# Kernel tuning notes

Hardware: AMD Instinct MI355X
Metric: run time of the kernel (lower is better)

The kernel has to match this reference:

```python
import jax, jax.numpy as jnp
import numpy as np

B, S, D, H, DQK, DV, DFF, L = 8, 512, 512, 8, 64, 64, 2048, 2
SCALE = float(np.sqrt(DQK))


def sinusoid_pe(s, d):
    pos = jnp.arange(s, dtype=jnp.float32)[:, None]
    div = jnp.exp(jnp.arange(0, d, 2, dtype=jnp.float32) * (-np.log(10000.0) / d))
    pe = jnp.zeros((s, d), jnp.float32)
    pe = pe.at[:, 0::2].set(jnp.sin(pos * div))
    pe = pe.at[:, 1::2].set(jnp.cos(pos * div))
    return pe


def ms_masks(s, steps=(4, 8, 16), rep=2):
    # Vectorized equivalent of multi_scale_mask: window of `step` neighbors,
    # shifted near the boundaries so the total neighbor count stays = step.
    i = jnp.arange(s)[:, None]
    j = jnp.arange(s)[None, :]
    ms = []
    for step in steps:
        s2 = step // 2
        left = jnp.where(i < s // 2, jnp.minimum(i, s2), step - jnp.minimum(s - 1 - i, s2))
        right = step - left
        m = (j >= i - left) & (j <= i + right)
        ms += [m] * rep
    return jnp.stack(ms)  # [6, S, S] bool


def layer_norm(x, g, b):
    mu = x.mean(-1, keepdims=True)
    var = ((x - mu) ** 2).mean(-1, keepdims=True)
    return (x - mu) / jnp.sqrt(var + 1e-6) * g + b


def mha(qin, kin, vin, wq, wk, wv, wo, g, b, mask):
    bq, lq, _ = qin.shape
    lk = kin.shape[1]
    q = (qin @ wq).reshape(bq, lq, H, DQK).transpose(0, 2, 1, 3)  # bhqd
    k = (kin @ wk).reshape(bq, lk, H, DQK).transpose(0, 2, 1, 3)
    v = (vin @ wv).reshape(bq, lk, H, DV).transpose(0, 2, 1, 3)
    scores = jnp.einsum('bhqd,bhkd->bhqk', q / SCALE, k)
    scores = jnp.where(mask, scores, jnp.float32(-1e9))
    p = jax.nn.softmax(scores, axis=-1)
    o = jnp.einsum('bhqk,bhkd->bhqd', p, v).transpose(0, 2, 1, 3).reshape(bq, lq, H * DV)
    return layer_norm(o @ wo + qin, g, b)


def ffn(x, w1, b1, w2, b2, g, bb):
    h = jax.nn.relu(x @ w1 + b1)
    return layer_norm(h @ w2 + b2 + x, g, bb)


def setup_inputs() -> dict:
    key = jax.random.key(0)
    ks = jax.random.split(key, 40)
    it = iter(range(40))
    d = {}
    d['src_seq'] = jax.random.normal(ks[next(it)], (B, S, D), jnp.float32)
    d['trg_seq'] = jax.random.normal(ks[next(it)], (B, S, D), jnp.float32)
    d['enc_pad_num'] = jax.random.randint(ks[next(it)], (B,), 0, 64)
    d['dec_pad_num'] = jax.random.randint(ks[next(it)], (B,), 0, 64)

    def w(shape):
        return jax.random.normal(ks[next(it)], shape, jnp.float32) * 0.02

    for p in ('e_wq', 'e_wk', 'e_wv'):
        d[p] = w((L, D, H * DQK))
    d['e_wo'] = w((L, H * DV, D))
    d['e_g1'] = jnp.ones((L, D)); d['e_b1'] = jnp.zeros((L, D))
    d['e_w1'] = w((L, D, DFF)); d['e_bb1'] = jnp.zeros((L, DFF))
    d['e_w2'] = w((L, DFF, D)); d['e_bb2'] = jnp.zeros((L, D))
    d['e_g2'] = jnp.ones((L, D)); d['e_b2'] = jnp.zeros((L, D))
    for p in ('d_swq', 'd_swk', 'd_swv'):
        d[p] = w((L, D, H * DQK))
    d['d_swo'] = w((L, H * DV, D))
    d['d_g1'] = jnp.ones((L, D)); d['d_b1'] = jnp.zeros((L, D))
    for p in ('d_cwq', 'd_cwk', 'd_cwv'):
        d[p] = w((L, D, H * DQK))
    d['d_cwo'] = w((L, H * DV, D))
    d['d_g2'] = jnp.ones((L, D)); d['d_b2'] = jnp.zeros((L, D))
    d['d_w1'] = w((L, D, DFF)); d['d_bb1'] = jnp.zeros((L, DFF))
    d['d_w2'] = w((L, DFF, D)); d['d_bb2'] = jnp.zeros((L, D))
    d['d_g3'] = jnp.ones((L, D)); d['d_b3'] = jnp.zeros((L, D))
    return d


def reference(src_seq, trg_seq, enc_pad_num, dec_pad_num,
              e_wq, e_wk, e_wv, e_wo, e_g1, e_b1, e_w1, e_bb1, e_w2, e_bb2, e_g2, e_b2,
              d_swq, d_swk, d_swv, d_swo, d_g1, d_b1,
              d_cwq, d_cwk, d_cwv, d_cwo, d_g2, d_b2,
              d_w1, d_bb1, d_w2, d_bb2, d_g3, d_b3):
    ms = ms_masks(S)  # [6, S, S]
    src_pad = jnp.arange(S)[None, :] < (S - enc_pad_num)[:, None]  # [B, S]
    trg_pad = jnp.arange(S)[None, :] < (S - dec_pad_num)[:, None]

    def full_mask(pad):
        base = pad[:, None, None, :]  # [B,1,1,S]
        win = jnp.logical_and(ms[None], base)  # [B,6,S,S]
        dense = jnp.broadcast_to(base, (B, H - ms.shape[0], S, S))
        return jnp.concatenate([win, dense], axis=1)  # [B,H,S,S]

    src_mask = full_mask(src_pad)
    trg_mask = full_mask(trg_pad)
    pe = sinusoid_pe(S, D)

    x = src_seq + pe[None]
    for l in range(L):
        x = mha(x, x, x, e_wq[l], e_wk[l], e_wv[l], e_wo[l], e_g1[l], e_b1[l], src_mask)
        x = ffn(x, e_w1[l], e_bb1[l], e_w2[l], e_bb2[l], e_g2[l], e_b2[l])

    y = trg_seq + pe[None]
    for l in range(L):
        y = mha(y, y, y, d_swq[l], d_swk[l], d_swv[l], d_swo[l], d_g1[l], d_b1[l], trg_mask)
        y = mha(y, x, x, d_cwq[l], d_cwk[l], d_cwv[l], d_cwo[l], d_g2[l], d_b2[l], src_mask)
        y = ffn(y, d_w1[l], d_bb1[l], d_w2[l], d_bb2[l], d_g3[l], d_b3[l])
    return y
```

## Files before the change

kernel.cpp:

```cpp
#include <hip/hip_runtime.h>
#include <hip/hip_bf16.h>

#define BB 8
#define SS 512
#define DD 512
#define HH 8
#define DQKv 64
#define DFFv 2048
#define LL 2

typedef __attribute__((ext_vector_type(8))) __bf16 bf16x8;
typedef __attribute__((ext_vector_type(4))) float f32x4;

static __device__ __forceinline__ ushort f2b(float x) {
    unsigned int u = __float_as_uint(x);
    unsigned int r = (u + 0x7FFFu + ((u >> 16) & 1u)) >> 16;
    return (ushort)r;
}
static __device__ __forceinline__ float b2f(ushort u) {
    return __uint_as_float(((unsigned int)u) << 16);
}

typedef __attribute__((address_space(1))) const unsigned int gas_u32;
typedef __attribute__((address_space(3))) unsigned int las_u32;
static __device__ __forceinline__ void gload16(const void* g, void* l) {
    __builtin_amdgcn_global_load_lds((gas_u32*)g, (las_u32*)l, 16, 0, 0);
}

__global__ __launch_bounds__(256) void add_pe2_k(const float* __restrict__ src,
                                                 const float* __restrict__ trg,
                                                 float* __restrict__ xf,
                                                 ushort* __restrict__ xb,
                                                 float* __restrict__ yf,
                                                 ushort* __restrict__ yb) {
    const int NQ = BB * SS * DD / 4;
    int i = blockIdx.x * 256 + threadIdx.x;
    const bool second = i >= NQ;
    const int ii = second ? i - NQ : i;
    const int rem = ii & (SS * DD / 4 - 1);
    const int d4 = rem & (DD / 4 - 1);
    const int s = rem >> 7;

    float4 a = ((const float4*)(second ? trg : src))[ii];
    const float c = -9.210340371976184f / 512.0f;
    const float div0 = __expf((float)(4 * d4) * c);
    const float div1 = __expf((float)(4 * d4 + 2) * c);
    const float a0 = (float)s * div0, a1 = (float)s * div1;
    a.x += sinf(a0); a.y += cosf(a0);
    a.z += sinf(a1); a.w += cosf(a1);

    float* of = second ? yf : xf;
    ushort* ob = second ? yb : xb;
    ((float4*)of)[ii] = a;
    ushort4 ub;
    ub.x = f2b(a.x); ub.y = f2b(a.y); ub.z = f2b(a.z); ub.w = f2b(a.w);
    ((ushort4*)ob)[ii] = ub;
}

__global__ __launch_bounds__(256) void tcast_k(const float* __restrict__ s0,
                                               const float* __restrict__ s1,
                                               const float* __restrict__ s2,
                                               const float* __restrict__ s3,
                                               ushort* __restrict__ dst,
                                               int K, int N) {
    __shared__ ushort st[64][72];
    const float* src = (blockIdx.z == 0) ? s0 : (blockIdx.z == 1) ? s1
                     : (blockIdx.z == 2) ? s2 : s3;
    ushort* d = dst + (size_t)blockIdx.z * K * N;
    const int k0 = blockIdx.y * 64, n0 = blockIdx.x * 64;
    const int t = threadIdx.x;
    const int r = t >> 2, c4 = (t & 3) * 16;
#pragma unroll
    for (int i = 0; i < 16; i += 4) {
        float4 v = *(const float4*)&src[(size_t)(k0 + r) * N + n0 + c4 + i];
        st[c4 + i + 0][r] = f2b(v.x);
        st[c4 + i + 1][r] = f2b(v.y);
        st[c4 + i + 2][r] = f2b(v.z);
        st[c4 + i + 3][r] = f2b(v.w);
    }
    __syncthreads();
    const int n = t >> 2, seg = (t & 3) * 16;
    *(uint4*)&d[(size_t)(n0 + n) * K + k0 + seg]     = *(const uint4*)&st[n][seg];
    *(uint4*)&d[(size_t)(n0 + n) * K + k0 + seg + 8] = *(const uint4*)&st[n][seg + 8];
}

#define NW 32
struct WTab {
    const float* src[NW];
    unsigned off[NW];
    int Kd[NW];
    int Nd[NW];
    int cum[NW + 1];
};

__global__ __launch_bounds__(256) void tcast_all_k(WTab tab, ushort* __restrict__ dst) {
    __shared__ ushort st[64][72];
    const int t = blockIdx.x;
    int m = 0;
    while (t >= tab.cum[m + 1]) ++m;
    const int local = t - tab.cum[m];
    const int ntx = tab.Nd[m];
    const int bx = local % ntx, by = local / ntx;
    const float* src = tab.src[m];
    ushort* d = dst + tab.off[m];
    const int N = ntx * 64, K = tab.Kd[m] * 64;
    const int k0 = by * 64, n0 = bx * 64;

    const int tt = threadIdx.x;
    const int r = tt >> 2, c4 = (tt & 3) * 16;
#pragma unroll
    for (int i = 0; i < 16; i += 4) {
        float4 v = *(const float4*)&src[(size_t)(k0 + r) * N + n0 + c4 + i];
        st[c4 + i + 0][r] = f2b(v.x);
        st[c4 + i + 1][r] = f2b(v.y);
        st[c4 + i + 2][r] = f2b(v.z);
        st[c4 + i + 3][r] = f2b(v.w);
    }
    __syncthreads();
    const int n = tt >> 2, seg = (tt & 3) * 16;
    *(uint4*)&d[(size_t)(n0 + n) * K + k0 + seg]     = *(const uint4*)&st[n][seg];
    *(uint4*)&d[(size_t)(n0 + n) * K + k0 + seg + 8] = *(const uint4*)&st[n][seg + 8];
}

template <bool BIAS, bool RES, bool RELU, bool OUTBF>
__global__ __launch_bounds__(256) void gemm2_k(const ushort* __restrict__ A,
                                               const ushort* __restrict__ Bt,
                                               const float* __restrict__ bias,
                                               const float* __restrict__ res,
                                               void* __restrict__ Cout,
                                               int M, int N, int K, int nbx) {
    __shared__ ushort sA[2][64 * 64];
    __shared__ ushort sB[2][64 * 64];

    const int tid = threadIdx.x;
    const int nwg = gridDim.x;
    const int wg = blockIdx.x;
    const int swz = (wg & 7) * (nwg >> 3) + (wg >> 3);
    const int bx = swz % nbx, by = swz / nbx;

    const int lane = tid & 63, w = tid >> 6;
    const int wm = w >> 1, wn = w & 1;
    const int llo = lane & 15, lhi = lane >> 4;

    const int srow = tid >> 3;
    const int scol = (((tid & 7) ^ (srow & 7)) * 8);
    const ushort* Ab = A + (size_t)(by * 64 + srow) * K + scol;
    const ushort* Bb = Bt + (size_t)(bx * 64 + srow) * K + scol;
    const int sOff = srow * 128 + (tid & 7) * 16;

    f32x4 acc[2][2] = {};
    const int nt = K >> 6;

#pragma unroll
    for (int i = 0; i < 2; ++i) {
        gload16(Ab + (size_t)i * 32 * K, (char*)sA[0] + sOff + i * 32 * 128);
        gload16(Bb + (size_t)i * 32 * K, (char*)sB[0] + sOff + i * 32 * 128);
    }
    __syncthreads();

    int cur = 0;
    for (int t = 0; t < nt; ++t) {
        if (t + 1 < nt) {
            const int k0 = (t + 1) << 6;
#pragma unroll
            for (int i = 0; i < 2; ++i) {
                gload16(Ab + (size_t)i * 32 * K + k0, (char*)sA[cur ^ 1] + sOff + i * 32 * 128);
                gload16(Bb + (size_t)i * 32 * K + k0, (char*)sB[cur ^ 1] + sOff + i * 32 * 128);
            }
        }
        const int sw = llo & 7;
#pragma unroll
        for (int ks = 0; ks < 2; ++ks) {
            const int pc = ((ks * 4 + lhi) ^ sw) * 8;
            bf16x8 af[2];
#pragma unroll
            for (int fa = 0; fa < 2; ++fa)
                af[fa] = *(const bf16x8*)&sA[cur][(wm * 32 + fa * 16 + llo) * 64 + pc];
            bf16x8 bfrag[2];
#pragma unroll
            for (int fb = 0; fb < 2; ++fb)
                bfrag[fb] = *(const bf16x8*)&sB[cur][(wn * 32 + fb * 16 + llo) * 64 + pc];
#pragma unroll
            for (int fa = 0; fa < 2; ++fa)
#pragma unroll
                for (int fb = 0; fb < 2; ++fb)
                    acc[fa][fb] = __builtin_amdgcn_mfma_f32_16x16x32_bf16(
                        af[fa], bfrag[fb], acc[fa][fb], 0, 0, 0);
        }
        __syncthreads();
        cur ^= 1;
    }

#pragma unroll
    for (int fa = 0; fa < 2; ++fa) {
#pragma unroll
        for (int fb = 0; fb < 2; ++fb) {
            const int col = bx * 64 + wn * 32 + fb * 16 + llo;
            const float bv = BIAS ? bias[col] : 0.f;
#pragma unroll
            for (int j = 0; j < 4; ++j) {
                const int row = by * 64 + wm * 32 + fa * 16 + lhi * 4 + j;
                float v = acc[fa][fb][j] + bv;
                if (RES) v += res[(size_t)row * N + col];
                if (RELU) v = fmaxf(v, 0.f);
                if (OUTBF) ((ushort*)Cout)[(size_t)row * N + col] = f2b(v);
                else       ((float*)Cout)[(size_t)row * N + col] = v;
            }
        }
    }
}

template <bool BIAS, bool RES, bool RELU, bool OUTBF>
__global__ __launch_bounds__(256) void gemm3_k(const ushort* __restrict__ A,
                                               const ushort* __restrict__ Bt,
                                               const float* __restrict__ bias,
                                               const float* __restrict__ res,
                                               void* __restrict__ Cout,
                                               int M, int N, int K, int nbx) {
    __shared__ ushort sA[2][64 * 64];
    __shared__ ushort sB[2][128 * 64];

    const int tid = threadIdx.x;
    const int nwg = gridDim.x;
    const int wg = blockIdx.x;
    const int swz = (wg & 7) * (nwg >> 3) + (wg >> 3);
    const int bx = swz % nbx, by = swz / nbx;

    const int lane = tid & 63, w = tid >> 6;
    const int wm = w >> 1, wn = w & 1;
    const int llo = lane & 15, lhi = lane >> 4;

    const int srow = tid >> 3;
    const int scol = (((tid & 7) ^ (srow & 7)) * 8);
    const ushort* Ab = A + (size_t)(by * 64 + srow) * K + scol;
    const ushort* Bb = Bt + (size_t)(bx * 128 + srow) * K + scol;
    const int sOff = srow * 128 + (tid & 7) * 16;

    f32x4 acc[2][4] = {};
    const int nt = K >> 6;

#pragma unroll
    for (int i = 0; i < 2; ++i)
        gload16(Ab + (size_t)i * 32 * K, (char*)sA[0] + sOff + i * 32 * 128);
#pragma unroll
    for (int i = 0; i < 4; ++i)
        gload16(Bb + (size_t)i * 32 * K, (char*)sB[0] + sOff + i * 32 * 128);
    __syncthreads();

    int cur = 0;
    for (int t = 0; t < nt; ++t) {
        if (t + 1 < nt) {
            const int k0 = (t + 1) << 6;
#pragma unroll
            for (int i = 0; i < 2; ++i)
                gload16(Ab + (size_t)i * 32 * K + k0, (char*)sA[cur ^ 1] + sOff + i * 32 * 128);
#pragma unroll
            for (int i = 0; i < 4; ++i)
                gload16(Bb + (size_t)i * 32 * K + k0, (char*)sB[cur ^ 1] + sOff + i * 32 * 128);
        }
        const int sw = llo & 7;
#pragma unroll
        for (int ks = 0; ks < 2; ++ks) {
            const int pc = ((ks * 4 + lhi) ^ sw) * 8;
            bf16x8 af[2];
#pragma unroll
            for (int fa = 0; fa < 2; ++fa)
                af[fa] = *(const bf16x8*)&sA[cur][(wm * 32 + fa * 16 + llo) * 64 + pc];
            bf16x8 bfrag[4];
#pragma unroll
            for (int fb = 0; fb < 4; ++fb)
                bfrag[fb] = *(const bf16x8*)&sB[cur][(wn * 64 + fb * 16 + llo) * 64 + pc];
#pragma unroll
            for (int fa = 0; fa < 2; ++fa)
#pragma unroll
                for (int fb = 0; fb < 4; ++fb)
                    acc[fa][fb] = __builtin_amdgcn_mfma_f32_16x16x32_bf16(
                        af[fa], bfrag[fb], acc[fa][fb], 0, 0, 0);
        }
        __syncthreads();
        cur ^= 1;
    }

#pragma unroll
    for (int fa = 0; fa < 2; ++fa) {
#pragma unroll
        for (int fb = 0; fb < 4; ++fb) {
            const int col = bx * 128 + wn * 64 + fb * 16 + llo;
            const float bv = BIAS ? bias[col] : 0.f;
#pragma unroll
            for (int j = 0; j < 4; ++j) {
                const int row = by * 64 + wm * 32 + fa * 16 + lhi * 4 + j;
                float v = acc[fa][fb][j] + bv;
                if (RES) v += res[(size_t)row * N + col];
                if (RELU) v = fmaxf(v, 0.f);
                if (OUTBF) ((ushort*)Cout)[(size_t)row * N + col] = f2b(v);
                else       ((float*)Cout)[(size_t)row * N + col] = v;
            }
        }
    }
}

__global__ __launch_bounds__(256) void attn_k(const ushort* __restrict__ QKV,
                                              ushort* __restrict__ O,
                                              const int* __restrict__ pad) {
    __shared__ ushort sQ[64][72];
    __shared__ ushort sK[64][72];
    __shared__ ushort sVt[64][72];
    __shared__ ushort sP[64][72];

    const int tid = threadIdx.x;
    const int b = blockIdx.z, h = blockIdx.y, q0 = blockIdx.x << 6;
    const int klim = SS - pad[b];
    const int lane = tid & 63, w = tid >> 6;
    const int qw0 = w << 4;
    const int lhi = lane >> 4, llo = lane & 15;
    const int ST = 3 * DD;

    {
        const int r = tid >> 2, seg = (tid & 3) << 4;
        const ushort* src = &QKV[(size_t)(b * SS + q0 + r) * ST + h * DQKv + seg];
        *(uint4*)&sQ[r][seg]     = *(const uint4*)src;
        *(uint4*)&sQ[r][seg + 8] = *(const uint4*)(src + 8);
    }

    auto window = [&](int i, int& wlo, int& whi) {
        if (h < 6) {
            const int step = 4 << (h >> 1);
            const int s2 = step >> 1;
            const int a1 = (i < s2) ? i : s2;
            const int a2 = ((SS - 1 - i) < s2) ? (SS - 1 - i) : s2;
            const int left = (i < SS / 2) ? a1 : (step - a2);
            wlo = i - left;
            whi = wlo + step;
        } else {
            wlo = 0;
            whi = SS - 1;
        }
    };

    int lo[4], hi[4];
#pragma unroll
    for (int j = 0; j < 4; ++j) window(q0 + qw0 + lhi * 4 + j, lo[j], hi[j]);

    int kt0 = 0, kt1 = SS;
    if (h < 6) {
        int lo0, hi0, lo63, hi63;
        window(q0, lo0, hi0);
        window(q0 + 63, lo63, hi63);
        if (lo63 >= klim) {
            kt0 = 0; kt1 = SS;
        } else {
            kt0 = (lo0 >> 6) << 6;
            kt1 = ((hi63 >> 6) + 1) << 6;
            if (kt1 > SS) kt1 = SS;
        }
    }

    float mr[4] = {-1e30f, -1e30f, -1e30f, -1e30f};
    float lr[4] = {0.f, 0.f, 0.f, 0.f};
    f32x4 oacc[4] = {};

    for (int kt = kt0; kt < kt1; kt += 64) {
        __syncthreads();
        {
            const int r = tid >> 2, seg = (tid & 3) << 4;
            const ushort* ksrc = &QKV[(size_t)(b * SS + kt + r) * ST + DD + h * DQKv + seg];
            *(uint4*)&sK[r][seg]     = *(const uint4*)ksrc;
            *(uint4*)&sK[r][seg + 8] = *(const uint4*)(ksrc + 8);
            const ushort* vsrc = &QKV[(size_t)(b * SS + kt + r) * ST + 2 * DD + h * DQKv + seg];
            uint4 u0 = *(const uint4*)vsrc;
            uint4 u1 = *(const uint4*)(vsrc + 8);
            const ushort* v0 = (const ushort*)&u0;
            const ushort* v1 = (const ushort*)&u1;
#pragma unroll
            for (int i = 0; i < 8; ++i) sVt[seg + i][r] = v0[i];
#pragma unroll
            for (int i = 0; i < 8; ++i) sVt[seg + 8 + i][r] = v1[i];
        }
        __syncthreads();

        f32x4 sacc[4] = {};
#pragma unroll
        for (int ks = 0; ks < 2; ++ks) {
            bf16x8 aq = *(const bf16x8*)&sQ[qw0 + llo][ks * 32 + lhi * 8];
#pragma unroll
            for (int n = 0; n < 4; ++n) {
                bf16x8 bk = *(const bf16x8*)&sK[n * 16 + llo][ks * 32 + lhi * 8];
                sacc[n] = __builtin_amdgcn_mfma_f32_16x16x32_bf16(aq, bk, sacc[n], 0, 0, 0);
            }
        }

#pragma unroll
        for (int j = 0; j < 4; ++j) {
            float s[4];
#pragma unroll
            for (int n = 0; n < 4; ++n) {
                const int kidx = kt + n * 16 + llo;
                const bool ok = (kidx < klim) && (kidx >= lo[j]) && (kidx <= hi[j]);
                s[n] = ok ? (sacc[n][j] * 0.125f) : -1e9f;
            }
            float tm = fmaxf(fmaxf(s[0], s[1]), fmaxf(s[2], s[3]));
#pragma unroll
            for (int off = 8; off; off >>= 1) tm = fmaxf(tm, __shfl_xor(tm, off));
            const float mn = fmaxf(mr[j], tm);
            const float alpha = __expf(mr[j] - mn);
            mr[j] = mn;
            float ps = 0.f;
            const int prow = qw0 + lhi * 4 + j;
#pragma unroll
            for (int n = 0; n < 4; ++n) {
                const ushort pb = f2b(__expf(s[n] - mn));
                sP[prow][n * 16 + llo] = pb;
                ps += b2f(pb);
            }
#pragma unroll
            for (int off = 8; off; off >>= 1) ps += __shfl_xor(ps, off);
            lr[j] = lr[j] * alpha + ps;
            oacc[0][j] *= alpha; oacc[1][j] *= alpha;
            oacc[2][j] *= alpha; oacc[3][j] *= alpha;
        }

#pragma unroll
        for (int ks = 0; ks < 2; ++ks) {
            bf16x8 ap = *(const bf16x8*)&sP[qw0 + llo][ks * 32 + lhi * 8];
#pragma unroll
            for (int n = 0; n < 4; ++n) {
                bf16x8 bv = *(const bf16x8*)&sVt[n * 16 + llo][ks * 32 + lhi * 8];
                oacc[n] = __builtin_amdgcn_mfma_f32_16x16x32_bf16(ap, bv, oacc[n], 0, 0, 0);
            }
        }
    }

#pragma unroll
    for (int j = 0; j < 4; ++j) {
        const float inv = 1.f / lr[j];
        const int q = q0 + qw0 + lhi * 4 + j;
#pragma unroll
        for (int n = 0; n < 4; ++n) {
            O[(size_t)(b * SS + q) * (HH * DQKv) + h * DQKv + n * 16 + llo] =
                f2b(oacc[n][j] * inv);
        }
    }
}

__global__ __launch_bounds__(256) void ln_k(const float* __restrict__ in,
                                            const float* __restrict__ g,
                                            const float* __restrict__ bvec,
                                            float* __restrict__ outf,
                                            ushort* __restrict__ outb) {
    const int row = blockIdx.x;
    const int tid = threadIdx.x;
    const float2 xv = *(const float2*)&in[(size_t)row * DD + tid * 2];

    __shared__ float red[4];
    __shared__ float red2[4];
    const int wid = tid >> 6, lane = tid & 63;

    float s = xv.x + xv.y;
#pragma unroll
    for (int off = 32; off; off >>= 1) s += __shfl_xor(s, off);
    if (lane == 0) red[wid] = s;
    __syncthreads();
    const float mu = (red[0] + red[1] + red[2] + red[3]) * (1.f / 512.f);

    const float dx = xv.x - mu, dy = xv.y - mu;
    float q = dx * dx + dy * dy;
#pragma unroll
    for (int off = 32; off; off >>= 1) q += __shfl_xor(q, off);
    if (lane == 0) red2[wid] = q;
    __syncthreads();
    const float var = (red2[0] + red2[1] + red2[2] + red2[3]) * (1.f / 512.f);
    const float rs = rsqrtf(var + 1e-6f);

    float2 o;
    o.x = dx * rs * g[tid * 2] + bvec[tid * 2];
    o.y = dy * rs * g[tid * 2 + 1] + bvec[tid * 2 + 1];
    *(float2*)&outf[(size_t)row * DD + tid * 2] = o;
    ushort2 ub; ub.x = f2b(o.x); ub.y = f2b(o.y);
    *(ushort2*)&outb[(size_t)row * DD + tid * 2] = ub;
}

extern "C" void kernel_launch(void* const* d_in, const int* in_sizes, int n_in,
                              void* d_out, int out_size, void* d_ws, size_t ws_size,
                              hipStream_t stream) {
    const float* src_seq = (const float*)d_in[0];
    const float* trg_seq = (const float*)d_in[1];
    const int* enc_pad = (const int*)d_in[2];
    const int* dec_pad = (const int*)d_in[3];
    const float* e_wq = (const float*)d_in[4];
    const float* e_wk = (const float*)d_in[5];
    const float* e_wv = (const float*)d_in[6];
    const float* e_wo = (const float*)d_in[7];
    const float* e_g1 = (const float*)d_in[8];
    const float* e_b1 = (const float*)d_in[9];
    const float* e_w1 = (const float*)d_in[10];
    const float* e_bb1 = (const float*)d_in[11];
    const float* e_w2 = (const float*)d_in[12];
    const float* e_bb2 = (const float*)d_in[13];
    const float* e_g2 = (const float*)d_in[14];
    const float* e_b2 = (const float*)d_in[15];
    const float* d_swq = (const float*)d_in[16];
    const float* d_swk = (const float*)d_in[17];
    const float* d_swv = (const float*)d_in[18];
    const float* d_swo = (const float*)d_in[19];
    const float* d_g1 = (const float*)d_in[20];
    const float* d_b1 = (const float*)d_in[21];
    const float* d_cwq = (const float*)d_in[22];
    const float* d_cwk = (const float*)d_in[23];
    const float* d_cwv = (const float*)d_in[24];
    const float* d_cwo = (const float*)d_in[25];
    const float* d_g2 = (const float*)d_in[26];
    const float* d_b2 = (const float*)d_in[27];
    const float* d_w1 = (const float*)d_in[28];
    const float* d_bb1 = (const float*)d_in[29];
    const float* d_w2 = (const float*)d_in[30];
    const float* d_bb2 = (const float*)d_in[31];
    const float* d_g3 = (const float*)d_in[32];
    const float* d_b3 = (const float*)d_in[33];
    (void)in_sizes; (void)n_in; (void)out_size;

    const int M = BB * SS;
    const int NTOK = BB * SS * DD;
    const size_t WSZ = (size_t)DD * 512;

    float* ws = (float*)d_ws;
    float* x  = ws;
    float* y  = x + NTOK;
    float* t0 = y + NTOK;
    ushort* xbf  = (ushort*)(t0 + NTOK);
    ushort* ybf  = xbf + NTOK;
    ushort* qkvb = ybf + NTOK;
    ushort* ob   = qkvb + (size_t)M * 1536;
    ushort* hbf  = qkvb;
    ushort* warena = ob + NTOK;

    const float* wsrc[NW]; int wK[NW], wN[NW]; size_t woff[NW];
    int wcnt = 0; size_t acc = 0;
    auto push = [&](const float* p, int K, int N) {
        wsrc[wcnt] = p; wK[wcnt] = K; wN[wcnt] = N; woff[wcnt] = acc;
        acc += (size_t)K * N; ++wcnt;
    };
    for (int l = 0; l < LL; ++l) {
        push(e_wq + (size_t)l * WSZ, 512, 512);
        push(e_wk + (size_t)l * WSZ, 512, 512);
        push(e_wv + (size_t)l * WSZ, 512, 512);
        push(e_wo + (size_t)l * WSZ, 512, 512);
        push(e_w1 + (size_t)l * DD * DFFv, 512, DFFv);
        push(e_w2 + (size_t)l * DFFv * DD, DFFv, 512);
    }
    for (int l = 0; l < LL; ++l) {
        push(d_swq + (size_t)l * WSZ, 512, 512);
        push(d_swk + (size_t)l * WSZ, 512, 512);
        push(d_swv + (size_t)l * WSZ, 512, 512);
        push(d_swo + (size_t)l * WSZ, 512, 512);
        push(d_cwq + (size_t)l * WSZ, 512, 512);
        push(d_cwk + (size_t)l * WSZ, 512, 512);
        push(d_cwv + (size_t)l * WSZ, 512, 512);
        push(d_cwo + (size_t)l * WSZ, 512, 512);
        push(d_w1 + (size_t)l * DD * DFFv, 512, DFFv);
        push(d_w2 + (size_t)l * DFFv * DD, DFFv, 512);
    }

    const size_t base_bytes = (size_t)(warena - (ushort*)d_ws) * 2;
    const bool big = ws_size >= base_bytes + acc * 2;

    if (big) {
        WTab tab;
        int tiles = 0;
        for (int i = 0; i < NW; ++i) {
            tab.src[i] = wsrc[i];
            tab.off[i] = (unsigned)woff[i];
            tab.Kd[i] = wK[i] / 64;
            tab.Nd[i] = wN[i] / 64;
            tab.cum[i] = tiles;
            tiles += (wK[i] / 64) * (wN[i] / 64);
        }
        tab.cum[NW] = tiles;
        tcast_all_k<<<tiles, 256, 0, stream>>>(tab, warena);
    }

    add_pe2_k<<<2 * NTOK / 4 / 256, 256, 0, stream>>>(src_seq, trg_seq, x, xbf, y, ybf);

    auto do_mha = [&](float* statef, ushort* statebf, const ushort* kvbf, int widx,
                      const float* g, const float* bb, const int* pad) {
        const ushort* bt;
        if (big) {
            bt = warena + woff[widx];
        } else {
            tcast_k<<<dim3(8, 8, 4), 256, 0, stream>>>(
                wsrc[widx], wsrc[widx + 1], wsrc[widx + 2], wsrc[widx + 3],
                warena, 512, 512);
            bt = warena;
        }
        if (kvbf == statebf) {
            gemm3_k<false, false, false, true><<<64 * 12, 256, 0, stream>>>(
                statebf, bt, nullptr, nullptr, qkvb, M, 1536, 512, 12);
        } else {
            gemm2_k<false, false, false, true><<<64 * 8, 256, 0, stream>>>(
                statebf, bt + 0 * WSZ, nullptr, nullptr, qkvb, M, 1536, 512, 8);
            gemm3_k<false, false, false, true><<<64 * 8, 256, 0, stream>>>(
                kvbf, bt + 1 * WSZ, nullptr, nullptr, qkvb + DD, M, 1536, 512, 8);
        }
        attn_k<<<dim3(SS / 64, HH, BB), 256, 0, stream>>>(qkvb, ob, pad);
        gemm2_k<false, true, false, false><<<64 * 8, 256, 0, stream>>>(
            ob, bt + 3 * WSZ, nullptr, statef, t0, M, 512, 512, 8);
        ln_k<<<M, 256, 0, stream>>>(t0, g, bb, statef, statebf);
    };
    auto do_ffn = [&](float* statef, ushort* statebf, int widx,
                      const float* b1, const float* b2,
                      const float* g, const float* bb, float* lnoutf) {
        const ushort* bt1;
        const ushort* bt2;
        if (big) {
            bt1 = warena + woff[widx];
            bt2 = warena + woff[widx + 1];
        } else {
            tcast_k<<<dim3(32, 8, 1), 256, 0, stream>>>(
                wsrc[widx], wsrc[widx], wsrc[widx], wsrc[widx], warena, 512, DFFv);
            bt1 = warena;
            bt2 = warena;
        }
        gemm3_k<true, false, true, true><<<64 * 16, 256, 0, stream>>>(
            statebf, bt1, b1, nullptr, hbf, M, DFFv, 512, 16);
        if (!big) {
            tcast_k<<<dim3(8, 32, 1), 256, 0, stream>>>(
                wsrc[widx + 1], wsrc[widx + 1], wsrc[widx + 1], wsrc[widx + 1],
                warena, DFFv, 512);
        }
        gemm2_k<true, true, false, false><<<64 * 8, 256, 0, stream>>>(
            hbf, bt2, b2, statef, t0, M, 512, DFFv, 8);
        ln_k<<<M, 256, 0, stream>>>(t0, g, bb, lnoutf, statebf);
    };

    for (int l = 0; l < LL; ++l) {
        do_mha(x, xbf, xbf, l * 6, e_g1 + l * DD, e_b1 + l * DD, enc_pad);
        do_ffn(x, xbf, l * 6 + 4, e_bb1 + l * DFFv, e_bb2 + l * DD,
               e_g2 + l * DD, e_b2 + l * DD, x);
    }
    for (int l = 0; l < LL; ++l) {
        do_mha(y, ybf, ybf, 12 + l * 10, d_g1 + l * DD, d_b1 + l * DD, dec_pad);
        do_mha(y, ybf, xbf, 12 + l * 10 + 4, d_g2 + l * DD, d_b2 + l * DD, enc_pad);
        const bool last = (l == LL - 1);
        do_ffn(y, ybf, 12 + l * 10 + 8, d_bb1 + l * DFFv, d_bb2 + l * DD,
               d_g3 + l * DD, d_b3 + l * DD, last ? (float*)d_out : y);
    }
}
```

Measured before the change: 593.7 us.

## Use triple-buffered LDS pipeline with explicit vmcnt waits in GEMM kernels

The 64x64 GEMM moves from a double-buffered to a triple-buffered LDS ring, prefetching two K-tiles ahead. Each iteration uses an explicit s_waitcnt vmcnt plus a single barrier instead of a full __syncthreads after compute. The 64x128 GEMM keeps double buffering but swaps __syncthreads for fine-grained vmcnt waits and sched barriers, so global-to-LDS loads overlap the MFMA work. Both rely on hand-counted vmcnt values matching the number of outstanding loads, which is fragile if the compiler emits other vector memory ops. The extra buffer also raises LDS use per block, which may lower occupancy.

```diff
diff --git a/kernel.cpp b/kernel.cpp
--- a/kernel.cpp
+++ b/kernel.cpp
@@ -26,6 +26,13 @@
 static __device__ __forceinline__ void gload16(const void* g, void* l) {
     __builtin_amdgcn_global_load_lds((gas_u32*)g, (las_u32*)l, 16, 0, 0);
 }
+
+#define VMCNT4 asm volatile("s_waitcnt vmcnt(4)" ::: "memory")
+#define VMCNT6 asm volatile("s_waitcnt vmcnt(6)" ::: "memory")
+#define VMCNT0 asm volatile("s_waitcnt vmcnt(0)" ::: "memory")
+#define LGKM0  asm volatile("s_waitcnt lgkmcnt(0)" ::: "memory")
+#define SCHEDB __builtin_amdgcn_sched_barrier(0)
+#define SBAR   __builtin_amdgcn_s_barrier()
 
 __global__ __launch_bounds__(256) void add_pe2_k(const float* __restrict__ src,
                                                  const float* __restrict__ trg,
@@ -129,8 +136,8 @@
                                                const float* __restrict__ res,
                                                void* __restrict__ Cout,
                                                int M, int N, int K, int nbx) {
-    __shared__ ushort sA[2][64 * 64];
-    __shared__ ushort sB[2][64 * 64];
+    __shared__ ushort sA[3][64 * 64];
+    __shared__ ushort sB[3][64 * 64];
 
     const int tid = threadIdx.x;
     const int nwg = gridDim.x;
@@ -156,18 +163,34 @@
         gload16(Ab + (size_t)i * 32 * K, (char*)sA[0] + sOff + i * 32 * 128);
         gload16(Bb + (size_t)i * 32 * K, (char*)sB[0] + sOff + i * 32 * 128);
     }
-    __syncthreads();
-
-    int cur = 0;
+    if (nt > 1) {
+#pragma unroll
+        for (int i = 0; i < 2; ++i) {
+            gload16(Ab + (size_t)i * 32 * K + 64, (char*)sA[1] + sOff + i * 32 * 128);
+            gload16(Bb + (size_t)i * 32 * K + 64, (char*)sB[1] + sOff + i * 32 * 128);
+        }
+    }
+    SCHEDB;
+
     for (int t = 0; t < nt; ++t) {
-        if (t + 1 < nt) {
-            const int k0 = (t + 1) << 6;
+        if (t + 1 < nt) { VMCNT4; } else { VMCNT0; }
+        LGKM0;
+        SCHEDB;
+        SBAR;
+        SCHEDB;
+        if (t + 2 < nt) {
+            const int k0 = (t + 2) << 6;
+            char* dA = (char*)sA[(t + 2) % 3] + sOff;
+            char* dB = (char*)sB[(t + 2) % 3] + sOff;
 #pragma unroll
             for (int i = 0; i < 2; ++i) {
-                gload16(Ab + (size_t)i * 32 * K + k0, (char*)sA[cur ^ 1] + sOff + i * 32 * 128);
-                gload16(Bb + (size_t)i * 32 * K + k0, (char*)sB[cur ^ 1] + sOff + i * 32 * 128);
+                gload16(Ab + (size_t)i * 32 * K + k0, dA + i * 32 * 128);
+                gload16(Bb + (size_t)i * 32 * K + k0, dB + i * 32 * 128);
             }
         }
+        SCHEDB;
+        const ushort* cA = sA[t % 3];
+        const ushort* cB = sB[t % 3];
         const int sw = llo & 7;
 #pragma unroll
         for (int ks = 0; ks < 2; ++ks) {
@@ -175,11 +198,11 @@
             bf16x8 af[2];
 #pragma unroll
             for (int fa = 0; fa < 2; ++fa)
-                af[fa] = *(const bf16x8*)&sA[cur][(wm * 32 + fa * 16 + llo) * 64 + pc];
+                af[fa] = *(const bf16x8*)&cA[(wm * 32 + fa * 16 + llo) * 64 + pc];
             bf16x8 bfrag[2];
 #pragma unroll
             for (int fb = 0; fb < 2; ++fb)
-                bfrag[fb] = *(const bf16x8*)&sB[cur][(wn * 32 + fb * 16 + llo) * 64 + pc];
+                bfrag[fb] = *(const bf16x8*)&cB[(wn * 32 + fb * 16 + llo) * 64 + pc];
 #pragma unroll
             for (int fa = 0; fa < 2; ++fa)
 #pragma unroll
@@ -187,8 +210,6 @@
                     acc[fa][fb] = __builtin_amdgcn_mfma_f32_16x16x32_bf16(
                         af[fa], bfrag[fb], acc[fa][fb], 0, 0, 0);
         }
-        __syncthreads();
-        cur ^= 1;
     }
 
 #pragma unroll
@@ -245,19 +266,29 @@
 #pragma unroll
     for (int i = 0; i < 4; ++i)
         gload16(Bb + (size_t)i * 32 * K, (char*)sB[0] + sOff + i * 32 * 128);
-    __syncthreads();
-
-    int cur = 0;
+    SCHEDB;
+
     for (int t = 0; t < nt; ++t) {
         if (t + 1 < nt) {
             const int k0 = (t + 1) << 6;
+            char* dA = (char*)sA[(t + 1) & 1] + sOff;
+            char* dB = (char*)sB[(t + 1) & 1] + sOff;
 #pragma unroll
             for (int i = 0; i < 2; ++i)
-                gload16(Ab + (size_t)i * 32 * K + k0, (char*)sA[cur ^ 1] + sOff + i * 32 * 128);
+                gload16(Ab + (size_t)i * 32 * K + k0, dA + i * 32 * 128);
 #pragma unroll
             for (int i = 0; i < 4; ++i)
-                gload16(Bb + (size_t)i * 32 * K + k0, (char*)sB[cur ^ 1] + sOff + i * 32 * 128);
-        }
+                gload16(Bb + (size_t)i * 32 * K + k0, dB + i * 32 * 128);
+            SCHEDB;
+            VMCNT6;
+        } else {
+            VMCNT0;
+        }
+        SCHEDB;
+        SBAR;
+        SCHEDB;
+        const ushort* cA = sA[t & 1];
+        const ushort* cB = sB[t & 1];
         const int sw = llo & 7;
 #pragma unroll
         for (int ks = 0; ks < 2; ++ks) {
@@ -265,11 +296,11 @@
             bf16x8 af[2];
 #pragma unroll
             for (int fa = 0; fa < 2; ++fa)
-                af[fa] = *(const bf16x8*)&sA[cur][(wm * 32 + fa * 16 + llo) * 64 + pc];
+                af[fa] = *(const bf16x8*)&cA[(wm * 32 + fa * 16 + llo) * 64 + pc];
             bf16x8 bfrag[4];
 #pragma unroll
             for (int fb = 0; fb < 4; ++fb)
-                bfrag[fb] = *(const bf16x8*)&sB[cur][(wn * 64 + fb * 16 + llo) * 64 + pc];
+                bfrag[fb] = *(const bf16x8*)&cB[(wn * 64 + fb * 16 + llo) * 64 + pc];
 #pragma unroll
             for (int fa = 0; fa < 2; ++fa)
 #pragma unroll
@@ -277,8 +308,9 @@
                     acc[fa][fb] = __builtin_amdgcn_mfma_f32_16x16x32_bf16(
                         af[fa], bfrag[fb], acc[fa][fb], 0, 0, 0);
         }
-        __syncthreads();
-        cur ^= 1;
+        LGKM0;
+        SCHEDB;
+        SBAR;
     }
 
 #pragma unroll
```

Result: no change. 588.2 us (-0.9%).
